# Performance work log

Hardware: AMD Instinct MI355X
Metric: run time of the kernel (lower is better)

Reference implementation:

```python
import jax, jax.numpy as jnp
import numpy as np

NUM_CLASSES = 14
ATTN_DIM = 64
BN_EPS = 1e-5

def setup_inputs() -> dict:
    key = jax.random.key(0)
    ks = jax.random.split(key, 6)
    B, F = 16384, 2048
    C, D = NUM_CLASSES, ATTN_DIM
    std = 0.02
    return {
        "features": jax.random.normal(ks[0], (B, F), jnp.float32),
        "W_proj": jax.random.normal(ks[1], (F, F), jnp.float32) * std,
        "b_proj": jnp.zeros((F,), jnp.float32),
        "bn_gamma": jnp.ones((F,), jnp.float32),
        "bn_beta": jnp.zeros((F,), jnp.float32),
        "W_qk": jax.random.normal(ks[2], (C * 2 * D, F), jnp.float32) * std,
        "gamma": jax.random.normal(ks[3], (C,), jnp.float32) * 0.1,
        "W_fc": jax.random.normal(ks[4], (C, F), jnp.float32) * std,
        "b_fc": jnp.zeros((C,), jnp.float32),
    }

def reference(features, W_proj, b_proj, bn_gamma, bn_beta, W_qk, gamma, W_fc, b_fc):
    B = features.shape[0]
    C, D = NUM_CLASSES, ATTN_DIM
    # fc logits
    logits = features @ W_fc.T + b_fc  # [B, C]
    # projection: Linear -> BatchNorm1d (training-mode batch stats) -> ReLU
    h = features @ W_proj.T + b_proj  # [B, P]
    mu = jnp.mean(h, axis=0)
    var = jnp.var(h, axis=0)  # biased, as torch BN uses for normalization
    h = (h - mu) * jax.lax.rsqrt(var + BN_EPS) * bn_gamma + bn_beta
    h = jax.nn.relu(h)
    # per-class q, k
    qk = h @ W_qk.T  # [B, 2*C*D]
    q, k = jnp.split(qk, 2, axis=-1)
    q = q.reshape(B, C, D)
    k = k.reshape(B, C, D)
    attn = jnp.einsum("bcd,bed->bce", q, k)  # [B, C, C]
    diag = jnp.diagonal(attn, axis1=-2, axis2=-1)  # [B, C]
    attn = attn - diag[..., None]
    attn = attn / jnp.max(jnp.abs(attn), axis=-1, keepdims=True)
    corr = jnp.einsum("bce,be->bc", attn, jax.nn.sigmoid(logits))  # [B, C]
    return logits + gamma * corr
```

## Files before the change

kernel.cpp:

```cpp
#include <hip/hip_runtime.h>
#include <stdint.h>


#define BROWS 16384
#define FDIM  2048
#define NCLS  14
#define ADIM  64
#define QKN   1792

typedef __attribute__((ext_vector_type(8))) short bhalf8_t;
typedef __attribute__((ext_vector_type(4))) float f32x4_t;

__device__ __forceinline__ unsigned short f2bf(float f) {
  unsigned int u = __builtin_bit_cast(unsigned int, f);
  u += 0x7fffu + ((u >> 16) & 1u);
  return (unsigned short)(u >> 16);
}
__device__ __forceinline__ float bf2f(unsigned short s) {
  return __builtin_bit_cast(float, (unsigned int)s << 16);
}

__device__ __forceinline__ void gl_lds16(const void* g, void* l) {
  __builtin_amdgcn_global_load_lds(
      (const __attribute__((address_space(1))) unsigned int*)g,
      (__attribute__((address_space(3))) unsigned int*)l, 16, 0, 0);
}

#define BAR() do { \
    asm volatile("" ::: "memory"); \
    __builtin_amdgcn_s_barrier(); \
    asm volatile("" ::: "memory"); \
  } while (0)

#define CN1 4194304
#define CN2 524288
#define CN3 458752
#define CN4 3584

__global__ void cast_all(const float* __restrict__ f, const float* __restrict__ wp,
                         const float* __restrict__ wqk, const float* __restrict__ wf,
                         unsigned short* __restrict__ dst) {
  int t = blockIdx.x * 256 + threadIdx.x;
  const float* src;
  if (t < CN1) src = f + (size_t)t * 8;
  else if (t < CN1 + CN2) src = wp + ((size_t)t - CN1) * 8;
  else if (t < CN1 + CN2 + CN3) src = wqk + ((size_t)t - CN1 - CN2) * 8;
  else src = wf + ((size_t)t - CN1 - CN2 - CN3) * 8;
  float4 a = ((const float4*)src)[0], b = ((const float4*)src)[1];
  bhalf8_t o;
  o[0] = f2bf(a.x); o[1] = f2bf(a.y); o[2] = f2bf(a.z); o[3] = f2bf(a.w);
  o[4] = f2bf(b.x); o[5] = f2bf(b.y); o[6] = f2bf(b.z); o[7] = f2bf(b.w);
  *((bhalf8_t*)dst + t) = o;
}

__global__ __launch_bounds__(256) void fc_logits(
    const unsigned short* __restrict__ featC, const unsigned short* __restrict__ WfC,
    const float* __restrict__ bfc, float* __restrict__ logits, float* __restrict__ colzero)
{
  __shared__ unsigned short lWf[NCLS * FDIM];
  if (blockIdx.x < 4)
    ((float4*)colzero)[blockIdx.x * 256 + (int)threadIdx.x] = (float4){0.f, 0.f, 0.f, 0.f};
  {
    const bhalf8_t* s = (const bhalf8_t*)WfC;
    bhalf8_t* d = (bhalf8_t*)lWf;
#pragma unroll
    for (int k = 0; k < 14; ++k)
      d[k * 256 + (int)threadIdx.x] = s[k * 256 + (int)threadIdx.x];
  }
  __syncthreads();

  const int lane = threadIdx.x & 63, wv = threadIdx.x >> 6;
  const int rbase = blockIdx.x * 16 + wv * 4;
  float acc[4][NCLS];
#pragma unroll
  for (int i = 0; i < 4; ++i)
#pragma unroll
    for (int c = 0; c < NCLS; ++c) acc[i][c] = 0.f;

#pragma unroll
  for (int w = 0; w < 4; ++w) {
    const int c8 = (w * 64 + lane) * 8;
    float fv[4][8];
#pragma unroll
    for (int i = 0; i < 4; ++i) {
      bhalf8_t fr = *(const bhalf8_t*)(featC + (size_t)(rbase + i) * FDIM + c8);
#pragma unroll
      for (int j = 0; j < 8; ++j) fv[i][j] = bf2f((unsigned short)fr[j]);
    }
#pragma unroll
    for (int c = 0; c < NCLS; ++c) {
      bhalf8_t wr = *(const bhalf8_t*)&lWf[c * FDIM + c8];
      float wv8[8];
#pragma unroll
      for (int j = 0; j < 8; ++j) wv8[j] = bf2f((unsigned short)wr[j]);
#pragma unroll
      for (int i = 0; i < 4; ++i) {
        float s = acc[i][c];
#pragma unroll
        for (int j = 0; j < 8; ++j) s += fv[i][j] * wv8[j];
        acc[i][c] = s;
      }
    }
  }
#pragma unroll
  for (int i = 0; i < 4; ++i)
#pragma unroll
    for (int c = 0; c < NCLS; ++c) {
      float v = acc[i][c];
      v += __shfl_xor(v, 1, 64);  v += __shfl_xor(v, 2, 64);
      v += __shfl_xor(v, 4, 64);  v += __shfl_xor(v, 8, 64);
      v += __shfl_xor(v, 16, 64); v += __shfl_xor(v, 32, 64);
      acc[i][c] = v;
    }
  if (lane == 0) {
#pragma unroll
    for (int i = 0; i < 4; ++i)
#pragma unroll
      for (int c = 0; c < NCLS; ++c)
        logits[(size_t)(rbase + i) * 16 + c] = acc[i][c] + bfc[c];
  }
}


template<int MODE>
__global__ __launch_bounds__(512, 2) void gemm256_bt(
    const unsigned short* __restrict__ A, const unsigned short* __restrict__ Bw,
    const float* __restrict__ bp,
    unsigned short* __restrict__ Cb,
    float* __restrict__ colsum, float* __restrict__ colsq,
    int K, int lda, int ldb, int ldc, int nby)
{
  __shared__ unsigned short L[2][2][2][8192];

  const int t = threadIdx.x;
  const int lane = t & 63;
  const int wv = t >> 6;
  const int m = lane & 15, quad = lane >> 4;
  const int wm = wv >> 2, wn = wv & 3;

  const int nwg = gridDim.x;
  const int wg = ((blockIdx.x & 7) * (nwg >> 3)) + (blockIdx.x >> 3);
  const int bx = wg / nby;
  const int by = wg - bx * nby;
  const int rowBase = bx << 8;
  const int colBase = by << 8;

  const int bO = (wn & 1) << 12;
  const int ofs0 = m * 64 + ((quad ^ (m & 7)) << 3);
  const int ofs1 = ofs0 ^ 32;

  const int r0 = t >> 3;
  const int q8 = ((t ^ r0) & 7) << 3;
  const int ldD = t << 3;
  const unsigned int aOff =
      (unsigned int)(rowBase + r0) * (unsigned int)lda + (unsigned int)q8;
  const unsigned int bOff00 = (unsigned int)(colBase + r0) * (unsigned int)ldb + q8;
  const unsigned int bOff01 = (unsigned int)(colBase + 64 + r0) * (unsigned int)ldb + q8;
  const unsigned int bOff10 = (unsigned int)(colBase + 128 + r0) * (unsigned int)ldb + q8;
  const unsigned int bOff11 = (unsigned int)(colBase + 192 + r0) * (unsigned int)ldb + q8;

#define STAGEA0(b, kb) do { \
    gl_lds16(A + aOff + (unsigned int)(kb), &L[b][0][0][ldD]); \
    gl_lds16(A + aOff + (unsigned int)(64 * lda) + (unsigned int)(kb), &L[b][0][0][ldD + 4096]); \
  } while (0)
#define STAGEA1(b, kb) do { \
    gl_lds16(A + aOff + (unsigned int)(128 * lda) + (unsigned int)(kb), &L[b][0][1][ldD]); \
    gl_lds16(A + aOff + (unsigned int)(192 * lda) + (unsigned int)(kb), &L[b][0][1][ldD + 4096]); \
  } while (0)
#define STAGEB0(b, kb) do { \
    gl_lds16(Bw + bOff00 + (unsigned int)(kb), &L[b][1][0][ldD]); \
    gl_lds16(Bw + bOff01 + (unsigned int)(kb), &L[b][1][0][ldD + 4096]); \
  } while (0)
#define STAGEB1(b, kb) do { \
    gl_lds16(Bw + bOff10 + (unsigned int)(kb), &L[b][1][1][ldD]); \
    gl_lds16(Bw + bOff11 + (unsigned int)(kb), &L[b][1][1][ldD + 4096]); \
  } while (0)

#define RDA(v, roff) \
    v##_0 = *(const bhalf8_t*)&LA[(roff) + ofs0]; \
    v##_1 = *(const bhalf8_t*)&LA[(roff) + ofs1];
#define RDB(v, roff) \
    v##_0 = *(const bhalf8_t*)&LB[(roff) + ofs0]; \
    v##_1 = *(const bhalf8_t*)&LB[(roff) + ofs1];
#define MM(i, j, av, bv) \
    acc[i][j] = __builtin_amdgcn_mfma_f32_16x16x32_bf16(av##_0, bv##_0, acc[i][j], 0, 0, 0); \
    acc[i][j] = __builtin_amdgcn_mfma_f32_16x16x32_bf16(av##_1, bv##_1, acc[i][j], 0, 0, 0);

  f32x4_t acc[8][4];
#pragma unroll
  for (int i = 0; i < 8; ++i)
#pragma unroll
    for (int j = 0; j < 4; ++j) acc[i][j] = (f32x4_t){0.f, 0.f, 0.f, 0.f};

  const int NT = K >> 6;

  STAGEA0(0, 0);
  STAGEA1(0, 0);
  STAGEB0(0, 0);
  STAGEB1(0, 0);
  {
    const int kb1 = (NT > 1) ? 64 : 0;
    STAGEB0(1, kb1);
    STAGEB1(1, kb1);
  }
  asm volatile("s_waitcnt vmcnt(4)" ::: "memory");
  BAR();

  for (int u = 0; u < NT; ++u) {
    const int buf = u & 1;
    const unsigned short* LA = &L[buf][0][wm][0];
    const unsigned short* LB = &L[buf][1][wn >> 1][bO];
    const int kbA = (u + 1 < NT) ? (u + 1) << 6 : 0;
    const int kbB = (u + 2 < NT) ? (u + 2) << 6 : 0;

    bhalf8_t a0_0, a0_1, a1_0, a1_1, a2_0, a2_1, a3_0, a3_1;
    bhalf8_t b0_0, b0_1, b1_0, b1_1, b2_0, b2_1, b3_0, b3_1;

    RDB(b0, 0);     RDB(b1, 1024);  RDB(b2, 2048);  RDB(b3, 3072);
    RDA(a0, 0);     RDA(a1, 1024);
    if (buf) { STAGEA0(0, kbA); } else { STAGEA0(1, kbA); }
    __builtin_amdgcn_s_setprio(1);
    MM(0, 0, a0, b0); MM(0, 1, a0, b1); MM(0, 2, a0, b2); MM(0, 3, a0, b3);
    MM(1, 0, a1, b0); MM(1, 1, a1, b1); MM(1, 2, a1, b2); MM(1, 3, a1, b3);
    __builtin_amdgcn_s_setprio(0);
    RDA(a2, 2048);  RDA(a3, 3072);
    if (buf) { STAGEA1(0, kbA); } else { STAGEA1(1, kbA); }
    BAR();

    __builtin_amdgcn_s_setprio(1);
    MM(2, 0, a2, b0); MM(2, 1, a2, b1); MM(2, 2, a2, b2); MM(2, 3, a2, b3);
    MM(3, 0, a3, b0); MM(3, 1, a3, b1); MM(3, 2, a3, b2); MM(3, 3, a3, b3);
    __builtin_amdgcn_s_setprio(0);
    RDA(a0, 4096);  RDA(a1, 5120);
    if (buf) { STAGEB0(1, kbB); } else { STAGEB0(0, kbB); }
    BAR();

    __builtin_amdgcn_s_setprio(1);
    MM(4, 0, a0, b0); MM(4, 1, a0, b1); MM(4, 2, a0, b2); MM(4, 3, a0, b3);
    MM(5, 0, a1, b0); MM(5, 1, a1, b1); MM(5, 2, a1, b2); MM(5, 3, a1, b3);
    __builtin_amdgcn_s_setprio(0);
    RDA(a2, 6144);  RDA(a3, 7168);
    if (buf) { STAGEB1(1, kbB); } else { STAGEB1(0, kbB); }
    BAR();

    __builtin_amdgcn_s_setprio(1);
    MM(6, 0, a2, b0); MM(6, 1, a2, b1); MM(6, 2, a2, b2); MM(6, 3, a2, b3);
    MM(7, 0, a3, b0); MM(7, 1, a3, b1); MM(7, 2, a3, b2); MM(7, 3, a3, b3);
    __builtin_amdgcn_s_setprio(0);
    asm volatile("s_waitcnt vmcnt(4)" ::: "memory");
    BAR();
  }
  asm volatile("s_waitcnt vmcnt(0)" ::: "memory");
  BAR();

#undef STAGEA0
#undef STAGEA1
#undef STAGEB0
#undef STAGEB1
#undef RDA
#undef RDB
#undef MM

  unsigned short* Lc = &L[0][0][0][0];
  if (MODE == 0) {
#pragma unroll
    for (int ni = 0; ni < 4; ++ni) {
      const int lcol = wn * 64 + ni * 16 + m;
      const int gcol = colBase + lcol;
      const float bv = bp[gcol];
      float s = 0.f, qq = 0.f;
#pragma unroll
      for (int mi = 0; mi < 8; ++mi) {
        const int lrow0 = wm * 128 + mi * 16 + quad * 4;
#pragma unroll
        for (int r = 0; r < 4; ++r) {
          float v = acc[mi][ni][r] + bv;
          const int lrow = lrow0 + r;
          Lc[lrow * 256 + (lcol ^ ((lrow & 7) << 3))] = f2bf(v);
          s += v; qq += v * v;
        }
      }
      s += __shfl_xor(s, 16, 64); s += __shfl_xor(s, 32, 64);
      qq += __shfl_xor(qq, 16, 64); qq += __shfl_xor(qq, 32, 64);
      if (quad == 0) { atomicAdd(&colsum[gcol], s); atomicAdd(&colsq[gcol], qq); }
    }
  } else {
#pragma unroll
    for (int ni = 0; ni < 4; ++ni) {
      const int lcol = wn * 64 + ni * 16 + m;
#pragma unroll
      for (int mi = 0; mi < 8; ++mi) {
        const int lrow0 = wm * 128 + mi * 16 + quad * 4;
#pragma unroll
        for (int r = 0; r < 4; ++r) {
          const int lrow = lrow0 + r;
          Lc[lrow * 256 + (lcol ^ ((lrow & 7) << 3))] = f2bf(acc[mi][ni][r]);
        }
      }
    }
  }
  asm volatile("s_waitcnt lgkmcnt(0)" ::: "memory");
  BAR();
#pragma unroll
  for (int i = 0; i < 16; ++i) {
    const int s = i * 512 + t;
    const int tr = s >> 5;
    const int c16 = s & 31;
    bhalf8_t vv = *(const bhalf8_t*)&Lc[tr * 256 + ((c16 ^ (tr & 7)) << 3)];
    *(bhalf8_t*)&Cb[(size_t)(rowBase + tr) * (size_t)ldc + (size_t)(colBase + (c16 << 3))] = vv;
  }
}

__global__ void bn_apply(unsigned short* __restrict__ hb,
                         const float* __restrict__ cs, const float* __restrict__ cq,
                         const float* __restrict__ g, const float* __restrict__ bt) {
  int t = blockIdx.x * 256 + threadIdx.x;
  int c8 = (t & 255) << 3;
  int row0 = t >> 8;
  const float inv = 1.f / (float)BROWS;
  float scv[8], shv[8];
#pragma unroll
  for (int j = 0; j < 8; ++j) {
    float mu = cs[c8 + j] * inv;
    float va = cq[c8 + j] * inv - mu * mu;
    float s = g[c8 + j] * rsqrtf(va + 1e-5f);
    scv[j] = s;
    shv[j] = bt[c8 + j] - mu * s;
  }
#pragma unroll
  for (int rr = 0; rr < 4; ++rr) {
    unsigned short* p = hb + (size_t)(row0 + rr * 4096) * FDIM + c8;
    bhalf8_t v = *(bhalf8_t*)p;
    bhalf8_t o;
#pragma unroll
    for (int j = 0; j < 8; ++j)
      o[j] = f2bf(fmaxf(bf2f((unsigned short)v[j]) * scv[j] + shv[j], 0.f));
    *(bhalf8_t*)p = o;
  }
}

__global__ __launch_bounds__(256) void attn_ep(
    const unsigned short* __restrict__ qk, const float* __restrict__ logits,
    const float* __restrict__ gamma, float* __restrict__ out)
{
  const int lane = threadIdx.x & 63;
  const int wv = threadIdx.x >> 6;
  const int b = blockIdx.x * 4 + wv;
  const int m = lane & 15, quad = lane >> 4;
  const unsigned short* qrow = qk + (size_t)b * QKN;
  f32x4_t acc = (f32x4_t){0.f, 0.f, 0.f, 0.f};
#pragma unroll
  for (int ks = 0; ks < 2; ++ks) {
    bhalf8_t af = {0,0,0,0,0,0,0,0}, bf = {0,0,0,0,0,0,0,0};
    if (m < NCLS) {
      af = *(const bhalf8_t*)(qrow + m * 64 + ks * 32 + quad * 8);
      bf = *(const bhalf8_t*)(qrow + 896 + m * 64 + ks * 32 + quad * 8);
    }
    acc = __builtin_amdgcn_mfma_f32_16x16x32_bf16(af, bf, acc, 0, 0, 0);
  }
  float logit_e = (m < NCLS) ? logits[(size_t)b * 16 + m] : 0.f;
  float sig = 1.f / (1.f + __expf(-logit_e));
  float corr[4];
#pragma unroll
  for (int r = 0; r < 4; ++r) {
    int c = quad * 4 + r;
    float diag = __shfl(acc[r], (lane & 48) + c, 64);
    float a = acc[r] - diag;
    float av = (m < NCLS) ? fabsf(a) : 0.f;
    av = fmaxf(av, __shfl_xor(av, 1, 64));
    av = fmaxf(av, __shfl_xor(av, 2, 64));
    av = fmaxf(av, __shfl_xor(av, 4, 64));
    av = fmaxf(av, __shfl_xor(av, 8, 64));
    float v = (m < NCLS) ? (a / av) * sig : 0.f;
    v += __shfl_xor(v, 1, 64);
    v += __shfl_xor(v, 2, 64);
    v += __shfl_xor(v, 4, 64);
    v += __shfl_xor(v, 8, 64);
    corr[r] = v;
  }
  if (m == 0) {
#pragma unroll
    for (int r = 0; r < 4; ++r) {
      int c = quad * 4 + r;
      if (c < NCLS) {
        float lc = logits[(size_t)b * 16 + c];
        out[(size_t)b * NCLS + c] = lc + gamma[c] * corr[r];
      }
    }
  }
}


extern "C" void kernel_launch(void* const* d_in, const int* in_sizes, int n_in,
                              void* d_out, int out_size, void* d_ws, size_t ws_size,
                              hipStream_t stream) {
  const float* features = (const float*)d_in[0];
  const float* W_proj   = (const float*)d_in[1];
  const float* b_proj   = (const float*)d_in[2];
  const float* bn_gamma = (const float*)d_in[3];
  const float* bn_beta  = (const float*)d_in[4];
  const float* W_qk     = (const float*)d_in[5];
  const float* gamma    = (const float*)d_in[6];
  const float* W_fc     = (const float*)d_in[7];
  const float* b_fc     = (const float*)d_in[8];
  float* out = (float*)d_out;

  char* ws = (char*)d_ws;
  unsigned short* featC   = (unsigned short*)ws;
  unsigned short* WpC     = (unsigned short*)(ws + 67108864);
  unsigned short* WqkC    = (unsigned short*)(ws + 75497472);
  unsigned short* WfC     = (unsigned short*)(ws + 82837504);
  unsigned short* hbuf    = (unsigned short*)(ws + 82894848);
  unsigned short* qkC     = (unsigned short*)(ws + 150003712);
  float*          logitsB = (float*)(ws + 208723968);
  float*          colsum  = (float*)(ws + 209772544);
  float*          colsq   = (float*)(ws + 209780736);

  cast_all<<<20238, 256, 0, stream>>>(features, W_proj, W_qk, W_fc, featC);

  fc_logits<<<1024, 256, 0, stream>>>(featC, WfC, b_fc, logitsB, colsum);

  gemm256_bt<0><<<512, 512, 0, stream>>>(
      featC, WpC, b_proj, hbuf, colsum, colsq, FDIM, FDIM, FDIM, FDIM, 8);

  bn_apply<<<4096, 256, 0, stream>>>(hbuf, colsum, colsq, bn_gamma, bn_beta);

  gemm256_bt<1><<<448, 512, 0, stream>>>(
      hbuf, WqkC, nullptr, qkC, nullptr, nullptr, FDIM, FDIM, FDIM, QKN, 7);

  attn_ep<<<BROWS / 4, 256, 0, stream>>>(qkC, logitsB, gamma, out);
}
```

Measured before the change: 529.6 us.

## Fuse bf16 casts into fc-logits kernel and merge GEMM pipeline phases

Removes the standalone cast kernel. The fc-logits kernel now reads fp32 features directly, converts them to bf16 and writes featC as a side effect, and also casts W_fc into LDS and W_proj/W_qk in a grid-stride loop. This drops one launch and a second read of the bf16 features. Separately, the GEMM main loop goes from four barrier-separated phases per K-step to two, issuing all A reads and stages up front. That cuts barriers but raises register pressure and reduces interleaving of loads with MFMA.

```diff
diff --git a/kernel.cpp b/kernel.cpp
--- a/kernel.cpp
+++ b/kernel.cpp
@@ -32,44 +32,44 @@
     asm volatile("" ::: "memory"); \
   } while (0)
 
-#define CN1 4194304
+#define CVT8(o, x, y) do { \
+    o[0] = f2bf(x.x); o[1] = f2bf(x.y); o[2] = f2bf(x.z); o[3] = f2bf(x.w); \
+    o[4] = f2bf(y.x); o[5] = f2bf(y.y); o[6] = f2bf(y.z); o[7] = f2bf(y.w); \
+  } while (0)
+
 #define CN2 524288
 #define CN3 458752
-#define CN4 3584
-
-__global__ void cast_all(const float* __restrict__ f, const float* __restrict__ wp,
-                         const float* __restrict__ wqk, const float* __restrict__ wf,
-                         unsigned short* __restrict__ dst) {
-  int t = blockIdx.x * 256 + threadIdx.x;
-  const float* src;
-  if (t < CN1) src = f + (size_t)t * 8;
-  else if (t < CN1 + CN2) src = wp + ((size_t)t - CN1) * 8;
-  else if (t < CN1 + CN2 + CN3) src = wqk + ((size_t)t - CN1 - CN2) * 8;
-  else src = wf + ((size_t)t - CN1 - CN2 - CN3) * 8;
-  float4 a = ((const float4*)src)[0], b = ((const float4*)src)[1];
-  bhalf8_t o;
-  o[0] = f2bf(a.x); o[1] = f2bf(a.y); o[2] = f2bf(a.z); o[3] = f2bf(a.w);
-  o[4] = f2bf(b.x); o[5] = f2bf(b.y); o[6] = f2bf(b.z); o[7] = f2bf(b.w);
-  *((bhalf8_t*)dst + t) = o;
-}
-
-__global__ __launch_bounds__(256) void fc_logits(
-    const unsigned short* __restrict__ featC, const unsigned short* __restrict__ WfC,
-    const float* __restrict__ bfc, float* __restrict__ logits, float* __restrict__ colzero)
+#define WCH (CN2 + CN3)
+
+__global__ __launch_bounds__(256) void prep_fused(
+    const float* __restrict__ feat, const float* __restrict__ wp,
+    const float* __restrict__ wqk, const float* __restrict__ wf,
+    const float* __restrict__ bfc,
+    unsigned short* __restrict__ featC, unsigned short* __restrict__ WpC,
+    float* __restrict__ logits, float* __restrict__ colzero)
 {
   __shared__ unsigned short lWf[NCLS * FDIM];
+  const int tid = threadIdx.x;
   if (blockIdx.x < 4)
-    ((float4*)colzero)[blockIdx.x * 256 + (int)threadIdx.x] = (float4){0.f, 0.f, 0.f, 0.f};
-  {
-    const bhalf8_t* s = (const bhalf8_t*)WfC;
-    bhalf8_t* d = (bhalf8_t*)lWf;
-#pragma unroll
-    for (int k = 0; k < 14; ++k)
-      d[k * 256 + (int)threadIdx.x] = s[k * 256 + (int)threadIdx.x];
+    ((float4*)colzero)[blockIdx.x * 256 + tid] = (float4){0.f, 0.f, 0.f, 0.f};
+
+#pragma unroll
+  for (int k = 0; k < NCLS; ++k) {
+    const float* s = wf + (size_t)k * FDIM + tid * 8;
+    float4 x = ((const float4*)s)[0], y = ((const float4*)s)[1];
+    bhalf8_t o; CVT8(o, x, y);
+    *(bhalf8_t*)&lWf[k * FDIM + tid * 8] = o;
+  }
+
+  for (int i = blockIdx.x * 256 + tid; i < WCH; i += 262144) {
+    const float* s = (i < CN2) ? wp + (size_t)i * 8 : wqk + ((size_t)i - CN2) * 8;
+    float4 x = ((const float4*)s)[0], y = ((const float4*)s)[1];
+    bhalf8_t o; CVT8(o, x, y);
+    *((bhalf8_t*)WpC + i) = o;
   }
   __syncthreads();
 
-  const int lane = threadIdx.x & 63, wv = threadIdx.x >> 6;
+  const int lane = tid & 63, wv = tid >> 6;
   const int rbase = blockIdx.x * 16 + wv * 4;
   float acc[4][NCLS];
 #pragma unroll
@@ -83,9 +83,12 @@
     float fv[4][8];
 #pragma unroll
     for (int i = 0; i < 4; ++i) {
-      bhalf8_t fr = *(const bhalf8_t*)(featC + (size_t)(rbase + i) * FDIM + c8);
-#pragma unroll
-      for (int j = 0; j < 8; ++j) fv[i][j] = bf2f((unsigned short)fr[j]);
+      const float* s = feat + (size_t)(rbase + i) * FDIM + c8;
+      float4 x = ((const float4*)s)[0], y = ((const float4*)s)[1];
+      fv[i][0] = x.x; fv[i][1] = x.y; fv[i][2] = x.z; fv[i][3] = x.w;
+      fv[i][4] = y.x; fv[i][5] = y.y; fv[i][6] = y.z; fv[i][7] = y.w;
+      bhalf8_t o; CVT8(o, x, y);
+      *(bhalf8_t*)(featC + (size_t)(rbase + i) * FDIM + c8) = o;
     }
 #pragma unroll
     for (int c = 0; c < NCLS; ++c) {
@@ -217,33 +220,23 @@
     bhalf8_t b0_0, b0_1, b1_0, b1_1, b2_0, b2_1, b3_0, b3_1;
 
     RDB(b0, 0);     RDB(b1, 1024);  RDB(b2, 2048);  RDB(b3, 3072);
-    RDA(a0, 0);     RDA(a1, 1024);
-    if (buf) { STAGEA0(0, kbA); } else { STAGEA0(1, kbA); }
+    RDA(a0, 0);     RDA(a1, 1024);  RDA(a2, 2048);  RDA(a3, 3072);
+    if (buf) { STAGEA0(0, kbA); STAGEA1(0, kbA); }
+    else     { STAGEA0(1, kbA); STAGEA1(1, kbA); }
     __builtin_amdgcn_s_setprio(1);
     MM(0, 0, a0, b0); MM(0, 1, a0, b1); MM(0, 2, a0, b2); MM(0, 3, a0, b3);
     MM(1, 0, a1, b0); MM(1, 1, a1, b1); MM(1, 2, a1, b2); MM(1, 3, a1, b3);
-    __builtin_amdgcn_s_setprio(0);
-    RDA(a2, 2048);  RDA(a3, 3072);
-    if (buf) { STAGEA1(0, kbA); } else { STAGEA1(1, kbA); }
-    BAR();
-
-    __builtin_amdgcn_s_setprio(1);
     MM(2, 0, a2, b0); MM(2, 1, a2, b1); MM(2, 2, a2, b2); MM(2, 3, a2, b3);
     MM(3, 0, a3, b0); MM(3, 1, a3, b1); MM(3, 2, a3, b2); MM(3, 3, a3, b3);
     __builtin_amdgcn_s_setprio(0);
-    RDA(a0, 4096);  RDA(a1, 5120);
-    if (buf) { STAGEB0(1, kbB); } else { STAGEB0(0, kbB); }
     BAR();
 
+    RDA(a0, 4096);  RDA(a1, 5120);  RDA(a2, 6144);  RDA(a3, 7168);
+    if (buf) { STAGEB0(1, kbB); STAGEB1(1, kbB); }
+    else     { STAGEB0(0, kbB); STAGEB1(0, kbB); }
     __builtin_amdgcn_s_setprio(1);
     MM(4, 0, a0, b0); MM(4, 1, a0, b1); MM(4, 2, a0, b2); MM(4, 3, a0, b3);
     MM(5, 0, a1, b0); MM(5, 1, a1, b1); MM(5, 2, a1, b2); MM(5, 3, a1, b3);
-    __builtin_amdgcn_s_setprio(0);
-    RDA(a2, 6144);  RDA(a3, 7168);
-    if (buf) { STAGEB1(1, kbB); } else { STAGEB1(0, kbB); }
-    BAR();
-
-    __builtin_amdgcn_s_setprio(1);
     MM(6, 0, a2, b0); MM(6, 1, a2, b1); MM(6, 2, a2, b2); MM(6, 3, a2, b3);
     MM(7, 0, a3, b0); MM(7, 1, a3, b1); MM(7, 2, a3, b2); MM(7, 3, a3, b3);
     __builtin_amdgcn_s_setprio(0);
@@ -409,16 +402,14 @@
   unsigned short* featC   = (unsigned short*)ws;
   unsigned short* WpC     = (unsigned short*)(ws + 67108864);
   unsigned short* WqkC    = (unsigned short*)(ws + 75497472);
-  unsigned short* WfC     = (unsigned short*)(ws + 82837504);
   unsigned short* hbuf    = (unsigned short*)(ws + 82894848);
   unsigned short* qkC     = (unsigned short*)(ws + 150003712);
   float*          logitsB = (float*)(ws + 208723968);
   float*          colsum  = (float*)(ws + 209772544);
   float*          colsq   = (float*)(ws + 209780736);
 
-  cast_all<<<20238, 256, 0, stream>>>(features, W_proj, W_qk, W_fc, featC);
-
-  fc_logits<<<1024, 256, 0, stream>>>(featC, WfC, b_fc, logitsB, colsum);
+  prep_fused<<<1024, 256, 0, stream>>>(
+      features, W_proj, W_qk, W_fc, b_fc, featC, WpC, logitsB, colsum);
 
   gemm256_bt<0><<<512, 512, 0, stream>>>(
       featC, WpC, b_proj, hbuf, colsum, colsq, FDIM, FDIM, FDIM, FDIM, 8);
```

New measurement: 519.1 us. 1.02x faster.
